# Kernel tuning notes

Measured on AMD Instinct MI355X. Metric: run time of the kernel, lower is better.

Reference implementation:

```python
import jax, jax.numpy as jnp
import numpy as np

H = 4  # hidden_size
L = 2  # num_layers


def _lstm_cell(x, h, c, Wih, Whh, bih, bhh):
    # PyTorch gate order: input, forget, cell(g), output
    gates = x @ Wih.T + h @ Whh.T + (bih + bhh)  # [B, 4H]
    i, f, g, o = jnp.split(gates, 4, axis=-1)
    i = jax.nn.sigmoid(i)
    f = jax.nn.sigmoid(f)
    g = jnp.tanh(g)
    o = jax.nn.sigmoid(o)
    c_new = f * c + i * g
    h_new = o * jnp.tanh(c_new)
    return h_new, c_new


def setup_inputs() -> dict:
    key = jax.random.key(0)
    ks = jax.random.split(key, 24)
    B, S, D, T = 32768, 256, 8, 12
    s = 1.0 / np.sqrt(H)  # PyTorch LSTM init scale

    def u(k, shape):
        return jax.random.uniform(k, shape, jnp.float32, -s, s)

    inp = {
        "src": jax.random.normal(ks[0], (B, S, D), jnp.float32),
        "trg": jax.random.normal(ks[1], (B, T, 1), jnp.float32),
        # encoder LSTM (input_dim=8 -> H, then H -> H)
        "enc_Wih0": u(ks[2], (4 * H, D)), "enc_Whh0": u(ks[3], (4 * H, H)),
        "enc_bih0": u(ks[4], (4 * H,)), "enc_bhh0": u(ks[5], (4 * H,)),
        "enc_Wih1": u(ks[6], (4 * H, H)), "enc_Whh1": u(ks[7], (4 * H, H)),
        "enc_bih1": u(ks[8], (4 * H,)), "enc_bhh1": u(ks[9], (4 * H,)),
        # decoder LSTM (input_dim=1 -> H, then H -> H)
        "dec_Wih0": u(ks[10], (4 * H, 1)), "dec_Whh0": u(ks[11], (4 * H, H)),
        "dec_bih0": u(ks[12], (4 * H,)), "dec_bhh0": u(ks[13], (4 * H,)),
        "dec_Wih1": u(ks[14], (4 * H, H)), "dec_Whh1": u(ks[15], (4 * H, H)),
        "dec_bih1": u(ks[16], (4 * H,)), "dec_bhh1": u(ks[17], (4 * H,)),
        # fc: hidden -> 1
        "fc_W": u(ks[18], (1, H)), "fc_b": u(ks[19], (1,)),
    }
    return inp


def reference(src, trg,
              enc_Wih0, enc_Whh0, enc_bih0, enc_bhh0,
              enc_Wih1, enc_Whh1, enc_bih1, enc_bhh1,
              dec_Wih0, dec_Whh0, dec_bih0, dec_bhh0,
              dec_Wih1, dec_Whh1, dec_bih1, dec_bhh1,
              fc_W, fc_b):
    B, T = src.shape[0], trg.shape[1]
    enc_layers = [(enc_Wih0, enc_Whh0, enc_bih0, enc_bhh0),
                  (enc_Wih1, enc_Whh1, enc_bih1, enc_bhh1)]
    dec_layers = [(dec_Wih0, dec_Whh0, dec_bih0, dec_bhh0),
                  (dec_Wih1, dec_Whh1, dec_bih1, dec_bhh1)]

    def multi_step(layers, h, c, x):
        new_h, new_c, inp = [], [], x
        for l, p in enumerate(layers):
            hl, cl = _lstm_cell(inp, h[l], c[l], *p)
            new_h.append(hl); new_c.append(cl); inp = hl
        return jnp.stack(new_h), jnp.stack(new_c), inp

    # ---- encoder: scan over src time steps ----
    h0 = jnp.zeros((L, B, H), src.dtype)
    c0 = jnp.zeros((L, B, H), src.dtype)

    def enc_step(carry, x_t):
        h, c = carry
        h, c, _ = multi_step(enc_layers, h, c, x_t)
        return (h, c), None

    (h, c), _ = jax.lax.scan(enc_step, (h0, c0), jnp.swapaxes(src, 0, 1))

    x0 = trg[:, 0, :]  # [B, 1]

    def dec_step(carry, _):
        h, c, x = carry
        h, c, top = multi_step(dec_layers, h, c, x)
        pred = top @ fc_W.T + fc_b  # [B, 1]
        return (h, c, pred), pred

    _, preds = jax.lax.scan(dec_step, (h, c, x0), None, length=T - 1)  # [T-1, B, 1]
    outputs = jnp.concatenate([x0[None], preds], axis=0)  # [T, B, 1]
    return jnp.swapaxes(outputs, 0, 1)  # [B, T, 1]
```

## Files before the change

kernel.cpp:

```cpp
#include <hip/hip_runtime.h>

namespace {

constexpr int Sn = 256;
constexpr int Tn = 12;

typedef float v2f __attribute__((ext_vector_type(2)));

__device__ __forceinline__ v2f pkfma(v2f a, v2f b, v2f c) {
  return __builtin_elementwise_fma(a, b, c);
}

__device__ __forceinline__ float rcp_(float x) { return __builtin_amdgcn_rcpf(x); }
__device__ __forceinline__ float sigm_(float x) { return rcp_(1.0f + __expf(-x)); }
__device__ __forceinline__ float tanh_(float x) { return 1.0f - 2.0f * rcp_(__expf(2.0f * x) + 1.0f); }

template <int CTRL>
__device__ __forceinline__ float qperm(float v) {
  return __int_as_float(
      __builtin_amdgcn_mov_dpp(__float_as_int(v), CTRL, 0xF, 0xF, true));
}
constexpr int DPP_XOR1 = 0xB1;
constexpr int DPP_XOR2 = 0x4E;
constexpr int DPP_XOR3 = 0x1B;
constexpr int DPP_BC0 = 0x00;

__device__ __forceinline__ float unit_update(v2f g01, v2f g23, float& c) {
  float iv = sigm_(g01.x);
  float fv = sigm_(g01.y);
  float gv = tanh_(g23.x);
  float ov = sigm_(g23.y);
  c = fmaf(fv, c, iv * gv);
  return ov * tanh_(c);
}

__device__ __forceinline__ void quad_gather(float h, float* hg) {
  hg[0] = h;
  hg[1] = qperm<DPP_XOR1>(h);
  hg[2] = qperm<DPP_XOR2>(h);
  hg[3] = qperm<DPP_XOR3>(h);
}

__global__ __launch_bounds__(64) void seq2seq_kernel(
    const float* __restrict__ src, const float* __restrict__ trg,
    const float* __restrict__ eWih0, const float* __restrict__ eWhh0,
    const float* __restrict__ ebih0, const float* __restrict__ ebhh0,
    const float* __restrict__ eWih1, const float* __restrict__ eWhh1,
    const float* __restrict__ ebih1, const float* __restrict__ ebhh1,
    const float* __restrict__ dWih0, const float* __restrict__ dWhh0,
    const float* __restrict__ dbih0, const float* __restrict__ dbhh0,
    const float* __restrict__ dWih1, const float* __restrict__ dWhh1,
    const float* __restrict__ dbih1, const float* __restrict__ dbhh1,
    const float* __restrict__ fcW, const float* __restrict__ fcb,
    float* __restrict__ out) {
  const int gid = blockIdx.x * 64 + threadIdx.x;
  const int e = gid >> 2;
  const int u = gid & 3;

  const int ri = u, rf = 4 + u, rg = 8 + u, ro = 12 + u;

  v2f w0x01[8], w0x23[8], w0h01[4], w0h23[4];
  v2f w1i01[4], w1i23[4], w1h01[4], w1h23[4];
#pragma unroll
  for (int j = 0; j < 8; ++j) {
    w0x01[j] = v2f{eWih0[ri * 8 + j], eWih0[rf * 8 + j]};
    w0x23[j] = v2f{eWih0[rg * 8 + j], eWih0[ro * 8 + j]};
  }
#pragma unroll
  for (int k = 0; k < 4; ++k) {
    const int kc = u ^ k;
    w0h01[k] = v2f{eWhh0[ri * 4 + kc], eWhh0[rf * 4 + kc]};
    w0h23[k] = v2f{eWhh0[rg * 4 + kc], eWhh0[ro * 4 + kc]};
    w1i01[k] = v2f{eWih1[ri * 4 + kc], eWih1[rf * 4 + kc]};
    w1i23[k] = v2f{eWih1[rg * 4 + kc], eWih1[ro * 4 + kc]};
    w1h01[k] = v2f{eWhh1[ri * 4 + kc], eWhh1[rf * 4 + kc]};
    w1h23[k] = v2f{eWhh1[rg * 4 + kc], eWhh1[ro * 4 + kc]};
  }
  const v2f b0_01 = v2f{ebih0[ri] + ebhh0[ri], ebih0[rf] + ebhh0[rf]};
  const v2f b0_23 = v2f{ebih0[rg] + ebhh0[rg], ebih0[ro] + ebhh0[ro]};
  const v2f b1_01 = v2f{ebih1[ri] + ebhh1[ri], ebih1[rf] + ebhh1[rf]};
  const v2f b1_23 = v2f{ebih1[rg] + ebhh1[rg], ebih1[ro] + ebhh1[ro]};

  const float4* sp = (const float4*)(src + (size_t)e * (Sn * 8));

  float h0g[4] = {0, 0, 0, 0};
  float h1g[4] = {0, 0, 0, 0};
  float c0 = 0.0f, c1 = 0.0f;

  auto enc_step = [&](float4 xa, float4 xb) {
    float x[8] = {xa.x, xa.y, xa.z, xa.w, xb.x, xb.y, xb.z, xb.w};
    v2f a01 = b0_01, a23 = b0_23;
#pragma unroll
    for (int j = 0; j < 8; ++j) {
      v2f xx = v2f{x[j], x[j]};
      a01 = pkfma(xx, w0x01[j], a01);
      a23 = pkfma(xx, w0x23[j], a23);
    }
#pragma unroll
    for (int k = 0; k < 4; ++k) {
      v2f hh = v2f{h0g[k], h0g[k]};
      a01 = pkfma(hh, w0h01[k], a01);
      a23 = pkfma(hh, w0h23[k], a23);
    }
    float h0 = unit_update(a01, a23, c0);
    quad_gather(h0, h0g);

    a01 = b1_01;
    a23 = b1_23;
#pragma unroll
    for (int k = 0; k < 4; ++k) {
      v2f hh0 = v2f{h0g[k], h0g[k]};
      v2f hh1 = v2f{h1g[k], h1g[k]};
      a01 = pkfma(hh0, w1i01[k], a01);
      a23 = pkfma(hh0, w1i23[k], a23);
      a01 = pkfma(hh1, w1h01[k], a01);
      a23 = pkfma(hh1, w1h23[k], a23);
    }
    float h1 = unit_update(a01, a23, c1);
    quad_gather(h1, h1g);
  };

  float4 A[16], B[16];
#pragma unroll
  for (int j = 0; j < 16; ++j) A[j] = sp[j];
#pragma unroll
  for (int j = 0; j < 16; ++j) B[j] = sp[16 + j];

  for (int i = 0; i < 16; ++i) {
#pragma unroll
    for (int s = 0; s < 8; ++s) enc_step(A[2 * s], A[2 * s + 1]);
    if (i < 15) {
#pragma unroll
      for (int j = 0; j < 16; ++j) A[j] = sp[32 * (i + 1) + j];
    }
#pragma unroll
    for (int s = 0; s < 8; ++s) enc_step(B[2 * s], B[2 * s + 1]);
    if (i < 15) {
#pragma unroll
      for (int j = 0; j < 16; ++j) B[j] = sp[32 * (i + 1) + 16 + j];
    }
  }

  v2f dw0i01 = v2f{dWih0[ri], dWih0[rf]};
  v2f dw0i23 = v2f{dWih0[rg], dWih0[ro]};
  v2f dw0h01[4], dw0h23[4], dw1i01[4], dw1i23[4], dw1h01[4], dw1h23[4];
#pragma unroll
  for (int k = 0; k < 4; ++k) {
    const int kc = u ^ k;
    dw0h01[k] = v2f{dWhh0[ri * 4 + kc], dWhh0[rf * 4 + kc]};
    dw0h23[k] = v2f{dWhh0[rg * 4 + kc], dWhh0[ro * 4 + kc]};
    dw1i01[k] = v2f{dWih1[ri * 4 + kc], dWih1[rf * 4 + kc]};
    dw1i23[k] = v2f{dWih1[rg * 4 + kc], dWih1[ro * 4 + kc]};
    dw1h01[k] = v2f{dWhh1[ri * 4 + kc], dWhh1[rf * 4 + kc]};
    dw1h23[k] = v2f{dWhh1[rg * 4 + kc], dWhh1[ro * 4 + kc]};
  }
  const v2f db0_01 = v2f{dbih0[ri] + dbhh0[ri], dbih0[rf] + dbhh0[rf]};
  const v2f db0_23 = v2f{dbih0[rg] + dbhh0[rg], dbih0[ro] + dbhh0[ro]};
  const v2f db1_01 = v2f{dbih1[ri] + dbhh1[ri], dbih1[rf] + dbhh1[rf]};
  const v2f db1_23 = v2f{dbih1[rg] + dbhh1[rg], dbih1[ro] + dbhh1[ro]};
  float fcw[4];
#pragma unroll
  for (int k = 0; k < 4; ++k) fcw[k] = fcW[u ^ k];
  const float fcbv = fcb[0];

  float xv = trg[(size_t)e * Tn];
  if (u == 0) out[(size_t)e * Tn] = xv;

  for (int t = 1; t < Tn; ++t) {
    v2f xx = v2f{xv, xv};
    v2f a01 = pkfma(xx, dw0i01, db0_01);
    v2f a23 = pkfma(xx, dw0i23, db0_23);
#pragma unroll
    for (int k = 0; k < 4; ++k) {
      v2f hh = v2f{h0g[k], h0g[k]};
      a01 = pkfma(hh, dw0h01[k], a01);
      a23 = pkfma(hh, dw0h23[k], a23);
    }
    float h0 = unit_update(a01, a23, c0);
    quad_gather(h0, h0g);

    a01 = db1_01;
    a23 = db1_23;
#pragma unroll
    for (int k = 0; k < 4; ++k) {
      v2f hh0 = v2f{h0g[k], h0g[k]};
      v2f hh1 = v2f{h1g[k], h1g[k]};
      a01 = pkfma(hh0, dw1i01[k], a01);
      a23 = pkfma(hh0, dw1i23[k], a23);
      a01 = pkfma(hh1, dw1h01[k], a01);
      a23 = pkfma(hh1, dw1h23[k], a23);
    }
    float h1 = unit_update(a01, a23, c1);
    quad_gather(h1, h1g);

    float pred = fcbv;
#pragma unroll
    for (int k = 0; k < 4; ++k) pred = fmaf(h1g[k], fcw[k], pred);
    pred = qperm<DPP_BC0>(pred);
    if (u == 0) out[(size_t)e * Tn + t] = pred;
    xv = pred;
  }
}

}

extern "C" void kernel_launch(void* const* d_in, const int* in_sizes, int n_in,
                              void* d_out, int out_size, void* d_ws, size_t ws_size,
                              hipStream_t stream) {
  const float* src = (const float*)d_in[0];
  const float* trg = (const float*)d_in[1];
  const float* eWih0 = (const float*)d_in[2];
  const float* eWhh0 = (const float*)d_in[3];
  const float* ebih0 = (const float*)d_in[4];
  const float* ebhh0 = (const float*)d_in[5];
  const float* eWih1 = (const float*)d_in[6];
  const float* eWhh1 = (const float*)d_in[7];
  const float* ebih1 = (const float*)d_in[8];
  const float* ebhh1 = (const float*)d_in[9];
  const float* dWih0 = (const float*)d_in[10];
  const float* dWhh0 = (const float*)d_in[11];
  const float* dbih0 = (const float*)d_in[12];
  const float* dbhh0 = (const float*)d_in[13];
  const float* dWih1 = (const float*)d_in[14];
  const float* dWhh1 = (const float*)d_in[15];
  const float* dbih1 = (const float*)d_in[16];
  const float* dbhh1 = (const float*)d_in[17];
  const float* fcW = (const float*)d_in[18];
  const float* fcb = (const float*)d_in[19];
  float* out = (float*)d_out;

  const int B = 32768;
  const int lanes = B * 4;
  const int block = 64;
  const int grid = lanes / block;
  seq2seq_kernel<<<grid, block, 0, stream>>>(
      src, trg, eWih0, eWhh0, ebih0, ebhh0, eWih1, eWhh1, ebih1, ebhh1,
      dWih0, dWhh0, dbih0, dbhh0, dWih1, dWhh1, dbih1, dbhh1, fcW, fcb, out);
}
```

Measured before the change: 448.9 us.

## Prefold log2e into weights, precompute input projections, reorder layer-1 FMAs

Pre-scales all gate weights and biases by -log2(e) (or 2·log2(e) for the cell gate) so the activations call the hardware exp2 directly, with no per-call multiply. The layer-0 input projection for each timestep is computed in batches interleaved between recurrent steps, taking it off the dependency chain. Layer-1 h1 contributions are accumulated before h0 is ready to shorten the critical path. It also adds a launch-bounds occupancy hint of two, which may raise register pressure because extra projected-input registers are now held.

```diff
diff --git a/kernel.cpp b/kernel.cpp
--- a/kernel.cpp
+++ b/kernel.cpp
@@ -4,6 +4,7 @@
 
 constexpr int Sn = 256;
 constexpr int Tn = 12;
+constexpr float L2E = 1.44269504088896340736f;
 
 typedef float v2f __attribute__((ext_vector_type(2)));
 
@@ -12,8 +13,12 @@
 }
 
 __device__ __forceinline__ float rcp_(float x) { return __builtin_amdgcn_rcpf(x); }
-__device__ __forceinline__ float sigm_(float x) { return rcp_(1.0f + __expf(-x)); }
-__device__ __forceinline__ float tanh_(float x) { return 1.0f - 2.0f * rcp_(__expf(2.0f * x) + 1.0f); }
+
+#if __has_builtin(__builtin_amdgcn_exp2f)
+__device__ __forceinline__ float exp2_(float x) { return __builtin_amdgcn_exp2f(x); }
+#else
+__device__ __forceinline__ float exp2_(float x) { return __expf(x * 0.69314718055994530942f); }
+#endif
 
 template <int CTRL>
 __device__ __forceinline__ float qperm(float v) {
@@ -26,12 +31,13 @@
 constexpr int DPP_BC0 = 0x00;
 
 __device__ __forceinline__ float unit_update(v2f g01, v2f g23, float& c) {
-  float iv = sigm_(g01.x);
-  float fv = sigm_(g01.y);
-  float gv = tanh_(g23.x);
-  float ov = sigm_(g23.y);
+  float iv = rcp_(1.0f + exp2_(g01.x));
+  float fv = rcp_(1.0f + exp2_(g01.y));
+  float gv = fmaf(-2.0f, rcp_(exp2_(g23.x) + 1.0f), 1.0f);
+  float ov = rcp_(1.0f + exp2_(g23.y));
   c = fmaf(fv, c, iv * gv);
-  return ov * tanh_(c);
+  float th = fmaf(-2.0f, rcp_(exp2_(c * (2.0f * L2E)) + 1.0f), 1.0f);
+  return ov * th;
 }
 
 __device__ __forceinline__ void quad_gather(float h, float* hg) {
@@ -41,7 +47,7 @@
   hg[3] = qperm<DPP_XOR3>(h);
 }
 
-__global__ __launch_bounds__(64) void seq2seq_kernel(
+__global__ __launch_bounds__(64, 2) void seq2seq_kernel(
     const float* __restrict__ src, const float* __restrict__ trg,
     const float* __restrict__ eWih0, const float* __restrict__ eWhh0,
     const float* __restrict__ ebih0, const float* __restrict__ ebhh0,
@@ -59,27 +65,30 @@
 
   const int ri = u, rf = 4 + u, rg = 8 + u, ro = 12 + u;
 
+  const v2f s01 = v2f{-L2E, -L2E};
+  const v2f s23 = v2f{2.0f * L2E, -L2E};
+
   v2f w0x01[8], w0x23[8], w0h01[4], w0h23[4];
   v2f w1i01[4], w1i23[4], w1h01[4], w1h23[4];
 #pragma unroll
   for (int j = 0; j < 8; ++j) {
-    w0x01[j] = v2f{eWih0[ri * 8 + j], eWih0[rf * 8 + j]};
-    w0x23[j] = v2f{eWih0[rg * 8 + j], eWih0[ro * 8 + j]};
+    w0x01[j] = v2f{eWih0[ri * 8 + j], eWih0[rf * 8 + j]} * s01;
+    w0x23[j] = v2f{eWih0[rg * 8 + j], eWih0[ro * 8 + j]} * s23;
   }
 #pragma unroll
   for (int k = 0; k < 4; ++k) {
     const int kc = u ^ k;
-    w0h01[k] = v2f{eWhh0[ri * 4 + kc], eWhh0[rf * 4 + kc]};
-    w0h23[k] = v2f{eWhh0[rg * 4 + kc], eWhh0[ro * 4 + kc]};
-    w1i01[k] = v2f{eWih1[ri * 4 + kc], eWih1[rf * 4 + kc]};
-    w1i23[k] = v2f{eWih1[rg * 4 + kc], eWih1[ro * 4 + kc]};
-    w1h01[k] = v2f{eWhh1[ri * 4 + kc], eWhh1[rf * 4 + kc]};
-    w1h23[k] = v2f{eWhh1[rg * 4 + kc], eWhh1[ro * 4 + kc]};
-  }
-  const v2f b0_01 = v2f{ebih0[ri] + ebhh0[ri], ebih0[rf] + ebhh0[rf]};
-  const v2f b0_23 = v2f{ebih0[rg] + ebhh0[rg], ebih0[ro] + ebhh0[ro]};
-  const v2f b1_01 = v2f{ebih1[ri] + ebhh1[ri], ebih1[rf] + ebhh1[rf]};
-  const v2f b1_23 = v2f{ebih1[rg] + ebhh1[rg], ebih1[ro] + ebhh1[ro]};
+    w0h01[k] = v2f{eWhh0[ri * 4 + kc], eWhh0[rf * 4 + kc]} * s01;
+    w0h23[k] = v2f{eWhh0[rg * 4 + kc], eWhh0[ro * 4 + kc]} * s23;
+    w1i01[k] = v2f{eWih1[ri * 4 + kc], eWih1[rf * 4 + kc]} * s01;
+    w1i23[k] = v2f{eWih1[rg * 4 + kc], eWih1[ro * 4 + kc]} * s23;
+    w1h01[k] = v2f{eWhh1[ri * 4 + kc], eWhh1[rf * 4 + kc]} * s01;
+    w1h23[k] = v2f{eWhh1[rg * 4 + kc], eWhh1[ro * 4 + kc]} * s23;
+  }
+  const v2f b0_01 = v2f{ebih0[ri] + ebhh0[ri], ebih0[rf] + ebhh0[rf]} * s01;
+  const v2f b0_23 = v2f{ebih0[rg] + ebhh0[rg], ebih0[ro] + ebhh0[ro]} * s23;
+  const v2f b1_01 = v2f{ebih1[ri] + ebhh1[ri], ebih1[rf] + ebhh1[rf]} * s01;
+  const v2f b1_23 = v2f{ebih1[rg] + ebhh1[rg], ebih1[ro] + ebhh1[ro]} * s23;
 
   const float4* sp = (const float4*)(src + (size_t)e * (Sn * 8));
 
@@ -87,7 +96,11 @@
   float h1g[4] = {0, 0, 0, 0};
   float c0 = 0.0f, c1 = 0.0f;
 
-  auto enc_step = [&](float4 xa, float4 xb) {
+  v2f xA01[8], xA23[8], xB01[8], xB23[8];
+  float4 raw[16];
+
+  auto convert = [&](int r, v2f& o01, v2f& o23) {
+    float4 xa = raw[2 * r], xb = raw[2 * r + 1];
     float x[8] = {xa.x, xa.y, xa.z, xa.w, xb.x, xb.y, xb.z, xb.w};
     v2f a01 = b0_01, a23 = b0_23;
 #pragma unroll
@@ -96,6 +109,11 @@
       a01 = pkfma(xx, w0x01[j], a01);
       a23 = pkfma(xx, w0x23[j], a23);
     }
+    o01 = a01;
+    o23 = a23;
+  };
+
+  auto rstep = [&](v2f a01, v2f a23) {
 #pragma unroll
     for (int k = 0; k < 4; ++k) {
       v2f hh = v2f{h0g[k], h0g[k]};
@@ -105,59 +123,79 @@
     float h0 = unit_update(a01, a23, c0);
     quad_gather(h0, h0g);
 
-    a01 = b1_01;
-    a23 = b1_23;
-#pragma unroll
-    for (int k = 0; k < 4; ++k) {
-      v2f hh0 = v2f{h0g[k], h0g[k]};
-      v2f hh1 = v2f{h1g[k], h1g[k]};
-      a01 = pkfma(hh0, w1i01[k], a01);
-      a23 = pkfma(hh0, w1i23[k], a23);
-      a01 = pkfma(hh1, w1h01[k], a01);
-      a23 = pkfma(hh1, w1h23[k], a23);
-    }
-    float h1 = unit_update(a01, a23, c1);
+    v2f e01 = b1_01, e23 = b1_23;
+#pragma unroll
+    for (int k = 0; k < 4; ++k) {
+      v2f hh = v2f{h1g[k], h1g[k]};
+      e01 = pkfma(hh, w1h01[k], e01);
+      e23 = pkfma(hh, w1h23[k], e23);
+    }
+#pragma unroll
+    for (int k = 0; k < 4; ++k) {
+      v2f hh = v2f{h0g[k], h0g[k]};
+      e01 = pkfma(hh, w1i01[k], e01);
+      e23 = pkfma(hh, w1i23[k], e23);
+    }
+    float h1 = unit_update(e01, e23, c1);
     quad_gather(h1, h1g);
   };
 
-  float4 A[16], B[16];
-#pragma unroll
-  for (int j = 0; j < 16; ++j) A[j] = sp[j];
-#pragma unroll
-  for (int j = 0; j < 16; ++j) B[j] = sp[16 + j];
+#pragma unroll
+  for (int j = 0; j < 16; ++j) raw[j] = sp[j];
+#pragma unroll
+  for (int r = 0; r < 8; ++r) convert(r, xA01[r], xA23[r]);
+#pragma unroll
+  for (int j = 0; j < 16; ++j) raw[j] = sp[16 + j];
 
   for (int i = 0; i < 16; ++i) {
-#pragma unroll
-    for (int s = 0; s < 8; ++s) enc_step(A[2 * s], A[2 * s + 1]);
+    rstep(xA01[0], xA23[0]);
+    rstep(xA01[1], xA23[1]);
+    rstep(xA01[2], xA23[2]);
+    rstep(xA01[3], xA23[3]);
+    rstep(xA01[4], xA23[4]); convert(0, xB01[0], xB23[0]); convert(1, xB01[1], xB23[1]);
+    rstep(xA01[5], xA23[5]); convert(2, xB01[2], xB23[2]); convert(3, xB01[3], xB23[3]);
+    rstep(xA01[6], xA23[6]); convert(4, xB01[4], xB23[4]); convert(5, xB01[5], xB23[5]);
+    rstep(xA01[7], xA23[7]); convert(6, xB01[6], xB23[6]); convert(7, xB01[7], xB23[7]);
     if (i < 15) {
 #pragma unroll
-      for (int j = 0; j < 16; ++j) A[j] = sp[32 * (i + 1) + j];
-    }
-#pragma unroll
-    for (int s = 0; s < 8; ++s) enc_step(B[2 * s], B[2 * s + 1]);
+      for (int j = 0; j < 16; ++j) raw[j] = sp[32 * (i + 1) + j];
+    }
+    rstep(xB01[0], xB23[0]);
+    rstep(xB01[1], xB23[1]);
+    rstep(xB01[2], xB23[2]);
+    rstep(xB01[3], xB23[3]);
     if (i < 15) {
-#pragma unroll
-      for (int j = 0; j < 16; ++j) B[j] = sp[32 * (i + 1) + 16 + j];
-    }
-  }
-
-  v2f dw0i01 = v2f{dWih0[ri], dWih0[rf]};
-  v2f dw0i23 = v2f{dWih0[rg], dWih0[ro]};
+      rstep(xB01[4], xB23[4]); convert(0, xA01[0], xA23[0]); convert(1, xA01[1], xA23[1]);
+      rstep(xB01[5], xB23[5]); convert(2, xA01[2], xA23[2]); convert(3, xA01[3], xA23[3]);
+      rstep(xB01[6], xB23[6]); convert(4, xA01[4], xA23[4]); convert(5, xA01[5], xA23[5]);
+      rstep(xB01[7], xB23[7]); convert(6, xA01[6], xA23[6]); convert(7, xA01[7], xA23[7]);
+#pragma unroll
+      for (int j = 0; j < 16; ++j) raw[j] = sp[32 * (i + 1) + 16 + j];
+    } else {
+      rstep(xB01[4], xB23[4]);
+      rstep(xB01[5], xB23[5]);
+      rstep(xB01[6], xB23[6]);
+      rstep(xB01[7], xB23[7]);
+    }
+  }
+
+  v2f dw0i01 = v2f{dWih0[ri], dWih0[rf]} * s01;
+  v2f dw0i23 = v2f{dWih0[rg], dWih0[ro]} * s23;
   v2f dw0h01[4], dw0h23[4], dw1i01[4], dw1i23[4], dw1h01[4], dw1h23[4];
 #pragma unroll
   for (int k = 0; k < 4; ++k) {
     const int kc = u ^ k;
-    dw0h01[k] = v2f{dWhh0[ri * 4 + kc], dWhh0[rf * 4 + kc]};
-    dw0h23[k] = v2f{dWhh0[rg * 4 + kc], dWhh0[ro * 4 + kc]};
-    dw1i01[k] = v2f{dWih1[ri * 4 + kc], dWih1[rf * 4 + kc]};
-    dw1i23[k] = v2f{dWih1[rg * 4 + kc], dWih1[ro * 4 + kc]};
-    dw1h01[k] = v2f{dWhh1[ri * 4 + kc], dWhh1[rf * 4 + kc]};
-    dw1h23[k] = v2f{dWhh1[rg * 4 + kc], dWhh1[ro * 4 + kc]};
-  }
-  const v2f db0_01 = v2f{dbih0[ri] + dbhh0[ri], dbih0[rf] + dbhh0[rf]};
-  const v2f db0_23 = v2f{dbih0[rg] + dbhh0[rg], dbih0[ro] + dbhh0[ro]};
-  const v2f db1_01 = v2f{dbih1[ri] + dbhh1[ri], dbih1[rf] + dbhh1[rf]};
-  const v2f db1_23 = v2f{dbih1[rg] + dbhh1[rg], dbih1[ro] + dbhh1[ro]};
+    dw0h01[k] = v2f{dWhh0[ri * 4 + kc], dWhh0[rf * 4 + kc]} * s01;
+    dw0h23[k] = v2f{dWhh0[rg * 4 + kc], dWhh0[ro * 4 + kc]} * s23;
+    dw1i01[k] = v2f{dWih1[ri * 4 + kc], dWih1[rf * 4 + kc]} * s01;
+    dw1i23[k] = v2f{dWih1[rg * 4 + kc], dWih1[ro * 4 + kc]} * s23;
+    dw1h01[k] = v2f{dWhh1[ri * 4 + kc], dWhh1[rf * 4 + kc]} * s01;
+    dw1h23[k] = v2f{dWhh1[rg * 4 + kc], dWhh1[ro * 4 + kc]} * s23;
+  }
+  const v2f db0_01 = v2f{dbih0[ri] + dbhh0[ri], dbih0[rf] + dbhh0[rf]} * s01;
+  const v2f db0_23 = v2f{dbih0[rg] + dbhh0[rg], dbih0[ro] + dbhh0[ro]} * s23;
+  const v2f db1_01 = v2f{dbih1[ri] + dbhh1[ri], dbih1[rf] + dbhh1[rf]} * s01;
+  const v2f db1_23 = v2f{dbih1[rg] + dbhh1[rg], dbih1[ro] + dbhh1[ro]} * s23;
   float fcw[4];
 #pragma unroll
   for (int k = 0; k < 4; ++k) fcw[k] = fcW[u ^ k];
@@ -179,18 +217,20 @@
     float h0 = unit_update(a01, a23, c0);
     quad_gather(h0, h0g);
 
-    a01 = db1_01;
-    a23 = db1_23;
-#pragma unroll
-    for (int k = 0; k < 4; ++k) {
-      v2f hh0 = v2f{h0g[k], h0g[k]};
-      v2f hh1 = v2f{h1g[k], h1g[k]};
-      a01 = pkfma(hh0, dw1i01[k], a01);
-      a23 = pkfma(hh0, dw1i23[k], a23);
-      a01 = pkfma(hh1, dw1h01[k], a01);
-      a23 = pkfma(hh1, dw1h23[k], a23);
-    }
-    float h1 = unit_update(a01, a23, c1);
+    v2f e01 = db1_01, e23 = db1_23;
+#pragma unroll
+    for (int k = 0; k < 4; ++k) {
+      v2f hh = v2f{h1g[k], h1g[k]};
+      e01 = pkfma(hh, dw1h01[k], e01);
+      e23 = pkfma(hh, dw1h23[k], e23);
+    }
+#pragma unroll
+    for (int k = 0; k < 4; ++k) {
+      v2f hh = v2f{h0g[k], h0g[k]};
+      e01 = pkfma(hh, dw1i01[k], e01);
+      e23 = pkfma(hh, dw1i23[k], e23);
+    }
+    float h1 = unit_update(e01, e23, c1);
     quad_gather(h1, h1g);
 
     float pred = fcbv;
```

Result: slower. 517.1 us (+15.2%).
